# Performance work log

Hardware: AMD Instinct MI355X
Metric: run time of the kernel (lower is better)

Reference implementation:

```python
import jax, jax.numpy as jnp
import numpy as np
from jax import lax

B, T, D_IN, D_OUT = 8, 4096, 256, 256


def setup_inputs() -> dict:
    key = jax.random.key(0)
    k1, k2, k3, k4, k5 = jax.random.split(key, 5)
    bound_in = 1.0 / np.sqrt(D_IN)
    return {
        "inputs": jax.random.normal(k1, (B, T, D_IN), dtype=jnp.float32),
        "mask": jnp.zeros((B, T, 1), dtype=jnp.float32),
        "W_in": jax.random.uniform(k2, (D_OUT, D_IN), jnp.float32, -bound_in, bound_in),
        "b_in": jax.random.uniform(k3, (D_OUT,), jnp.float32, -bound_in, bound_in),
        "W_f": jax.random.uniform(k4, (D_OUT, D_IN), jnp.float32, -bound_in, bound_in),
        "b_f": jax.random.uniform(k5, (D_OUT,), jnp.float32, -bound_in, bound_in),
    }


def _forget_mult(f, x):
    # h_t = f_t * x_t + (1 - f_t) * h_{t-1}, h_{-1} = 0 (torchqrnn ForgetMult, hidden_init=None)
    fT = jnp.swapaxes(f, 0, 1)  # (T, B, D)
    xT = jnp.swapaxes(x, 0, 1)

    def step(h, fx):
        ft, xt = fx
        h = ft * xt + (1.0 - ft) * h
        return h, h

    h0 = jnp.zeros(xT.shape[1:], dtype=x.dtype)  # (B, D)
    _, hs = lax.scan(step, h0, (fT, xT))
    return jnp.swapaxes(hs, 0, 1)  # (B, T, D)


def reference(inputs, mask, W_in, b_in, W_f, b_f):
    # right_to_left = False -> no flips
    x = jnp.tanh(jnp.einsum("btd,od->bto", inputs, W_in) + b_in)
    f = jax.nn.sigmoid(jnp.einsum("btd,od->bto", inputs, W_f) + b_f + mask * 10000.0)
    return _forget_mult(f, x)
```

## Files before the change

### kernel.cpp

```cpp
#include <hip/hip_runtime.h>
#include <math.h>


typedef _Float16 f16x8 __attribute__((ext_vector_type(8)));
typedef float f32x4 __attribute__((ext_vector_type(4)));
typedef float f32x16 __attribute__((ext_vector_type(16)));

constexpr int B_ = 8, T_ = 4096, D_ = 256, K_ = 256;
constexpr int M_ = B_ * T_;
constexpr int CHUNK = 64;
constexpr int NCH = T_ / CHUNK;

struct alignas(4) XF { _Float16 x, f; };

__device__ __forceinline__ float fexp2(float a) { return __builtin_amdgcn_exp2f(a); }
__device__ __forceinline__ float frcp(float a) { return __builtin_amdgcn_rcpf(a); }
constexpr float L2E = 1.4426950408889634f;

__device__ __forceinline__ float fast_sigmoid(float z) {
  return frcp(1.f + fexp2(-z * L2E));
}
__device__ __forceinline__ float fast_tanh(float z) {
  const float t = fexp2(-2.f * L2E * fabsf(z));
  return copysignf((1.f - t) * frcp(1.f + t), z);
}

__global__ __launch_bounds__(256) void wconv(const float* __restrict__ Win,
                                             const float* __restrict__ Wf,
                                             _Float16* __restrict__ Wh2) {
  const int t = blockIdx.x * 256 + threadIdx.x;
  const int n = t & 255;
  const int kc = (t >> 8) & 3;
  const int mat = (t >> 10) & 1;
  const int kk = t >> 11;
  const float* s = (mat ? Wf : Win) + (size_t)n * K_ + kk * 32 + kc * 8;
  f32x4 a = *(const f32x4*)s;
  f32x4 b = *(const f32x4*)(s + 4);
  f16x8 o;
  o[0] = (_Float16)a[0]; o[1] = (_Float16)a[1];
  o[2] = (_Float16)a[2]; o[3] = (_Float16)a[3];
  o[4] = (_Float16)b[0]; o[5] = (_Float16)b[1];
  o[6] = (_Float16)b[2]; o[7] = (_Float16)b[3];
  *(f16x8*)(Wh2 + (size_t)t * 8) = o;
}

__global__ __launch_bounds__(256, 2) void gemm_fused(
    const float* __restrict__ A, const _Float16* __restrict__ Wh2,
    const float* __restrict__ bin, const float* __restrict__ bfv,
    const float* __restrict__ mask, XF* __restrict__ xf,
    float* __restrict__ Ap, float* __restrict__ Hp) {
  __shared__ __align__(16) char smem[65536];
  char* ldsA = smem;
  char* ldsW = smem + 32768;

  const int tid = threadIdx.x;
  const int w = tid >> 6, lane = tid & 63;
  const int mw = w >> 1, nw = w & 1;
  const int nl = lane & 31, kh = lane >> 5;
  const int ml = mw * 32 + nl;
  const int g = blockIdx.x;
  const int row0b = g * CHUNK;

  f32x16 acc[2][4];
#pragma unroll
  for (int mat = 0; mat < 2; ++mat)
#pragma unroll
    for (int nt = 0; nt < 4; ++nt) acc[mat][nt] = (f32x16)(0.f);

  {
    const int am = tid >> 2;
    const int ak4 = (tid & 3) * 8;
    const float* agp = A + (size_t)(row0b + am) * K_ + ak4 * 8;
#pragma unroll
    for (int j = 0; j < 8; ++j) {
      const int kcg = ak4 + j;
      f32x4 lo = *(const f32x4*)(agp + j * 8);
      f32x4 hi = *(const f32x4*)(agp + j * 8 + 4);
      f16x8 t;
      t[0] = (_Float16)lo[0]; t[1] = (_Float16)lo[1];
      t[2] = (_Float16)lo[2]; t[3] = (_Float16)lo[3];
      t[4] = (_Float16)hi[0]; t[5] = (_Float16)hi[1];
      t[6] = (_Float16)hi[2]; t[7] = (_Float16)hi[3];
      *(f16x8*)(ldsA + am * 512 + ((kcg ^ (am & 31)) << 4)) = t;
    }
  }

  f16x8 wreg[8];
#pragma unroll
  for (int j = 0; j < 8; ++j)
    wreg[j] = *(const f16x8*)(Wh2 + (size_t)(j * 256 + tid) * 8);

  for (int kk = 0; kk < 8; ++kk) {
#pragma unroll
    for (int j = 0; j < 8; ++j)
      *(f16x8*)(ldsW + (size_t)(j * 256 + tid) * 16) = wreg[j];
    __syncthreads();
    if (kk < 7) {
#pragma unroll
      for (int j = 0; j < 8; ++j)
        wreg[j] = *(const f16x8*)(Wh2 + (size_t)(kk + 1) * 16384 +
                                  (size_t)(j * 256 + tid) * 8);
    }
    f16x8 afr[2];
#pragma unroll
    for (int i2 = 0; i2 < 2; ++i2) {
      const int kcg = kk * 4 + i2 * 2 + kh;
      afr[i2] = *(const f16x8*)(ldsA + ml * 512 + ((kcg ^ (ml & 31)) << 4));
    }
#pragma unroll
    for (int mat = 0; mat < 2; ++mat)
#pragma unroll
      for (int nt = 0; nt < 4; ++nt) {
        const int n = nw * 128 + nt * 32 + nl;
#pragma unroll
        for (int i2 = 0; i2 < 2; ++i2) {
          const int kc = i2 * 2 + kh;
          f16x8 bfr = *(const f16x8*)(ldsW + (size_t)((mat * 4 + kc) * 256 + n) * 16);
          acc[mat][nt] = __builtin_amdgcn_mfma_f32_32x32x16_f16(
              afr[i2], bfr, acc[mat][nt], 0, 0, 0);
        }
      }
    __syncthreads();
  }

  float bx[4], bf[4];
#pragma unroll
  for (int nt = 0; nt < 4; ++nt) {
    const int col = nw * 128 + nt * 32 + nl;
    bx[nt] = bin[col];
    bf[nt] = bfv[col];
  }
  float madd[16];
  int rowl[16];
#pragma unroll
  for (int reg = 0; reg < 16; ++reg) {
    const int rl = mw * 32 + (reg & 3) + 8 * (reg >> 2) + 4 * kh;
    rowl[reg] = rl;
    madd[reg] = 10000.f * mask[row0b + rl];
  }
#pragma unroll
  for (int nt = 0; nt < 4; ++nt) {
    const int col = nw * 128 + nt * 32 + nl;
#pragma unroll
    for (int reg = 0; reg < 16; ++reg) {
      const float zx = acc[0][nt][reg] + bx[nt];
      const float zf = acc[1][nt][reg] + bf[nt] + madd[reg];
      XF v;
      v.x = (_Float16)fast_tanh(zx);
      v.f = (_Float16)fast_sigmoid(zf);
      *(XF*)(smem + ((size_t)rowl[reg] * D_ + col) * 4) = v;
      xf[((size_t)row0b + rowl[reg]) * D_ + col] = v;
    }
  }
  __syncthreads();

  const int d = tid;
  float Aa = 1.f, h = 0.f;
#pragma unroll 8
  for (int t = 0; t < CHUNK; ++t) {
    const XF v = *(const XF*)(smem + ((size_t)t * D_ + d) * 4);
    const float f = (float)v.f;
    const float a = 1.f - f;
    h = f * (float)v.x + a * h;
    Aa *= a;
  }
  Ap[(size_t)g * D_ + d] = Aa;
  Hp[(size_t)g * D_ + d] = h;
}

__global__ __launch_bounds__(256) void scan_final(const XF* __restrict__ xf,
                                                  const float* __restrict__ Ap,
                                                  const float* __restrict__ Hp,
                                                  float* __restrict__ out) {
  const int g = blockIdx.x;
  const int b = g >> 6, c = g & 63;
  const int d = threadIdx.x;
  const float* ap = Ap + ((size_t)b * NCH) * D_ + d;
  const float* hp = Hp + ((size_t)b * NCH) * D_ + d;
  float h = 0.f;
  for (int j = 0; j < c; ++j) h = hp[(size_t)j * D_] + ap[(size_t)j * D_] * h;

  const size_t base = (size_t)g * CHUNK * D_ + d;
#pragma unroll 8
  for (int t = 0; t < CHUNK; ++t) {
    const XF v = xf[base + (size_t)t * D_];
    const float f = (float)v.f;
    h = f * (float)v.x + (1.f - f) * h;
    out[base + (size_t)t * D_] = h;
  }
}

extern "C" void kernel_launch(void* const* d_in, const int* in_sizes, int n_in,
                              void* d_out, int out_size, void* d_ws, size_t ws_size,
                              hipStream_t stream) {
  const float* inputs = (const float*)d_in[0];
  const float* mask   = (const float*)d_in[1];
  const float* W_in   = (const float*)d_in[2];
  const float* b_in   = (const float*)d_in[3];
  const float* W_f    = (const float*)d_in[4];
  const float* b_f    = (const float*)d_in[5];
  float* out = (float*)d_out;
  char* ws = (char*)d_ws;

  constexpr size_t XFSZ = (size_t)M_ * D_ * sizeof(XF);
  constexpr size_t WSZ  = (size_t)2 * 256 * 256 * 2;
  constexpr size_t SUM  = (size_t)M_ / CHUNK * D_ * sizeof(float);

  XF* xf = (XF*)ws;
  _Float16* Wh2 = (_Float16*)(ws + XFSZ);
  float* Ap = (float*)(ws + XFSZ + WSZ);
  float* Hp = Ap + SUM / sizeof(float);

  wconv<<<64, 256, 0, stream>>>(W_in, W_f, Wh2);
  gemm_fused<<<512, 256, 0, stream>>>(inputs, Wh2, b_in, b_f, mask, xf, Ap, Hp);
  scan_final<<<512, 256, 0, stream>>>(xf, Ap, Hp, out);
}
```

Measured before the change: 129.9 us.

## Fuse chunk scan into GEMM kernel with cross-block flag-based carry propagation

Merges the separate scan_final kernel into the GEMM kernel. Each block publishes its chunk summary (decay product and partial state) with atomic stores and a release flag, waits on the flags of earlier chunks in the same batch, then rebuilds its carry-in and writes the output straight from LDS. This removes the fp16 x/f intermediate round trip through global memory and one kernel launch. In exchange it adds a memset, spin-waiting that relies on all 512 blocks being co-resident or scheduled in order, and serial latency along each batch's chain of chunks.

```diff
diff --git a/kernel.cpp b/kernel.cpp
--- a/kernel.cpp
+++ b/kernel.cpp
@@ -10,6 +10,7 @@
 constexpr int M_ = B_ * T_;
 constexpr int CHUNK = 64;
 constexpr int NCH = T_ / CHUNK;
+constexpr int NBLK = M_ / CHUNK;
 
 struct alignas(4) XF { _Float16 x, f; };
 
@@ -44,11 +45,11 @@
   *(f16x8*)(Wh2 + (size_t)t * 8) = o;
 }
 
-__global__ __launch_bounds__(256, 2) void gemm_fused(
+__global__ __launch_bounds__(256, 2) void gemm_scan(
     const float* __restrict__ A, const _Float16* __restrict__ Wh2,
     const float* __restrict__ bin, const float* __restrict__ bfv,
-    const float* __restrict__ mask, XF* __restrict__ xf,
-    float* __restrict__ Ap, float* __restrict__ Hp) {
+    const float* __restrict__ mask, unsigned long long* __restrict__ AH,
+    int* __restrict__ flags, float* __restrict__ out) {
   __shared__ __align__(16) char smem[65536];
   char* ldsA = smem;
   char* ldsW = smem + 32768;
@@ -149,41 +150,53 @@
       v.x = (_Float16)fast_tanh(zx);
       v.f = (_Float16)fast_sigmoid(zf);
       *(XF*)(smem + ((size_t)rowl[reg] * D_ + col) * 4) = v;
-      xf[((size_t)row0b + rowl[reg]) * D_ + col] = v;
     }
   }
   __syncthreads();
 
   const int d = tid;
-  float Aa = 1.f, h = 0.f;
+  {
+    float Aa = 1.f, h = 0.f;
+#pragma unroll 8
+    for (int t = 0; t < CHUNK; ++t) {
+      const XF v = *(const XF*)(smem + ((size_t)t * D_ + d) * 4);
+      const float f = (float)v.f;
+      const float a = 1.f - f;
+      h = f * (float)v.x + a * h;
+      Aa *= a;
+    }
+    union { float f2[2]; unsigned long long u; } pk;
+    pk.f2[0] = Aa; pk.f2[1] = h;
+    __hip_atomic_store(AH + (size_t)g * D_ + d, pk.u, __ATOMIC_RELAXED,
+                       __HIP_MEMORY_SCOPE_AGENT);
+  }
+  __syncthreads();
+  if (tid == 0)
+    __hip_atomic_store(flags + g, 1, __ATOMIC_RELEASE, __HIP_MEMORY_SCOPE_AGENT);
+
+  const int b = g >> 6, c = g & 63;
+  const int s0 = b << 6;
+  if (tid < c) {
+    while (__hip_atomic_load(flags + s0 + tid, __ATOMIC_ACQUIRE,
+                             __HIP_MEMORY_SCOPE_AGENT) == 0)
+      __builtin_amdgcn_s_sleep(8);
+  }
+  __syncthreads();
+
+  float h = 0.f;
+  for (int j = s0; j < g; ++j) {
+    unsigned long long u = __hip_atomic_load(AH + (size_t)j * D_ + d,
+                                             __ATOMIC_RELAXED,
+                                             __HIP_MEMORY_SCOPE_AGENT);
+    union { unsigned long long u; float f2[2]; } pk;
+    pk.u = u;
+    h = pk.f2[1] + pk.f2[0] * h;
+  }
+
+  const size_t base = (size_t)row0b * D_ + d;
 #pragma unroll 8
   for (int t = 0; t < CHUNK; ++t) {
     const XF v = *(const XF*)(smem + ((size_t)t * D_ + d) * 4);
-    const float f = (float)v.f;
-    const float a = 1.f - f;
-    h = f * (float)v.x + a * h;
-    Aa *= a;
-  }
-  Ap[(size_t)g * D_ + d] = Aa;
-  Hp[(size_t)g * D_ + d] = h;
-}
-
-__global__ __launch_bounds__(256) void scan_final(const XF* __restrict__ xf,
-                                                  const float* __restrict__ Ap,
-                                                  const float* __restrict__ Hp,
-                                                  float* __restrict__ out) {
-  const int g = blockIdx.x;
-  const int b = g >> 6, c = g & 63;
-  const int d = threadIdx.x;
-  const float* ap = Ap + ((size_t)b * NCH) * D_ + d;
-  const float* hp = Hp + ((size_t)b * NCH) * D_ + d;
-  float h = 0.f;
-  for (int j = 0; j < c; ++j) h = hp[(size_t)j * D_] + ap[(size_t)j * D_] * h;
-
-  const size_t base = (size_t)g * CHUNK * D_ + d;
-#pragma unroll 8
-  for (int t = 0; t < CHUNK; ++t) {
-    const XF v = xf[base + (size_t)t * D_];
     const float f = (float)v.f;
     h = f * (float)v.x + (1.f - f) * h;
     out[base + (size_t)t * D_] = h;
@@ -202,16 +215,15 @@
   float* out = (float*)d_out;
   char* ws = (char*)d_ws;
 
-  constexpr size_t XFSZ = (size_t)M_ * D_ * sizeof(XF);
-  constexpr size_t WSZ  = (size_t)2 * 256 * 256 * 2;
-  constexpr size_t SUM  = (size_t)M_ / CHUNK * D_ * sizeof(float);
-
-  XF* xf = (XF*)ws;
-  _Float16* Wh2 = (_Float16*)(ws + XFSZ);
-  float* Ap = (float*)(ws + XFSZ + WSZ);
-  float* Hp = Ap + SUM / sizeof(float);
-
+  constexpr size_t WSZ = (size_t)2 * 256 * 256 * 2;
+  constexpr size_t AHSZ = (size_t)NBLK * D_ * 8;
+
+  _Float16* Wh2 = (_Float16*)ws;
+  unsigned long long* AH = (unsigned long long*)(ws + WSZ);
+  int* flags = (int*)(ws + WSZ + AHSZ);
+
+  hipMemsetAsync(flags, 0, NBLK * sizeof(int), stream);
   wconv<<<64, 256, 0, stream>>>(W_in, W_f, Wh2);
-  gemm_fused<<<512, 256, 0, stream>>>(inputs, Wh2, b_in, b_f, mask, xf, Ap, Hp);
-  scan_final<<<512, 256, 0, stream>>>(xf, Ap, Hp, out);
-}
+  gemm_scan<<<NBLK, 256, 0, stream>>>(inputs, Wh2, b_in, b_f, mask, AH, flags,
+                                      out);
+}
```

Measured after the change: 136.9 us. +5.4%, slower.

## Shrink GEMM tile to 32 rows and read weights straight from global memory

Applied to the files above, without the earlier changes.

The fused GEMM now handles 32 rows per block instead of 64, which doubles the grid to 1024 blocks. The weight fragments are loaded straight from global memory (L2/L1) rather than staged through LDS with double-buffered registers. LDS use is halved and the occupancy hint rises to 3 blocks per CU, meant to improve latency hiding and parallelism. The trade-off is redundant weight reads per block. The final scan must also chain twice as many chunk summaries per block, since each 64-step output chunk now has two 32-row partial summaries.

```diff
diff --git a/kernel.cpp b/kernel.cpp
--- a/kernel.cpp
+++ b/kernel.cpp
@@ -8,6 +8,8 @@
 
 constexpr int B_ = 8, T_ = 4096, D_ = 256, K_ = 256;
 constexpr int M_ = B_ * T_;
+constexpr int GROWS = 32;
+constexpr int NGB = M_ / GROWS;
 constexpr int CHUNK = 64;
 constexpr int NCH = T_ / CHUNK;
 
@@ -44,36 +46,33 @@
   *(f16x8*)(Wh2 + (size_t)t * 8) = o;
 }
 
-__global__ __launch_bounds__(256, 2) void gemm_fused(
+__global__ __launch_bounds__(256, 3) void gemm32(
     const float* __restrict__ A, const _Float16* __restrict__ Wh2,
     const float* __restrict__ bin, const float* __restrict__ bfv,
     const float* __restrict__ mask, XF* __restrict__ xf,
     float* __restrict__ Ap, float* __restrict__ Hp) {
-  __shared__ __align__(16) char smem[65536];
+  __shared__ __align__(16) char smem[32768];
   char* ldsA = smem;
-  char* ldsW = smem + 32768;
 
   const int tid = threadIdx.x;
   const int w = tid >> 6, lane = tid & 63;
-  const int mw = w >> 1, nw = w & 1;
   const int nl = lane & 31, kh = lane >> 5;
-  const int ml = mw * 32 + nl;
   const int g = blockIdx.x;
-  const int row0b = g * CHUNK;
-
-  f32x16 acc[2][4];
+  const int row0 = g * GROWS;
+
+  f32x16 acc[2][2];
 #pragma unroll
   for (int mat = 0; mat < 2; ++mat)
 #pragma unroll
-    for (int nt = 0; nt < 4; ++nt) acc[mat][nt] = (f32x16)(0.f);
+    for (int nt = 0; nt < 2; ++nt) acc[mat][nt] = (f32x16)(0.f);
 
   {
-    const int am = tid >> 2;
-    const int ak4 = (tid & 3) * 8;
-    const float* agp = A + (size_t)(row0b + am) * K_ + ak4 * 8;
-#pragma unroll
-    for (int j = 0; j < 8; ++j) {
-      const int kcg = ak4 + j;
+    const int am = tid >> 3;
+    const int kb = (tid & 7) * 4;
+    const float* agp = A + (size_t)(row0 + am) * K_ + kb * 8;
+#pragma unroll
+    for (int j = 0; j < 4; ++j) {
+      const int kcg = kb + j;
       f32x4 lo = *(const f32x4*)(agp + j * 8);
       f32x4 hi = *(const f32x4*)(agp + j * 8 + 4);
       f16x8 t;
@@ -81,52 +80,40 @@
       t[2] = (_Float16)lo[2]; t[3] = (_Float16)lo[3];
       t[4] = (_Float16)hi[0]; t[5] = (_Float16)hi[1];
       t[6] = (_Float16)hi[2]; t[7] = (_Float16)hi[3];
-      *(f16x8*)(ldsA + am * 512 + ((kcg ^ (am & 31)) << 4)) = t;
+      *(f16x8*)(ldsA + am * 512 + ((kcg ^ am) << 4)) = t;
     }
   }
-
-  f16x8 wreg[8];
-#pragma unroll
-  for (int j = 0; j < 8; ++j)
-    wreg[j] = *(const f16x8*)(Wh2 + (size_t)(j * 256 + tid) * 8);
-
+  __syncthreads();
+
+#pragma unroll 2
   for (int kk = 0; kk < 8; ++kk) {
-#pragma unroll
-    for (int j = 0; j < 8; ++j)
-      *(f16x8*)(ldsW + (size_t)(j * 256 + tid) * 16) = wreg[j];
-    __syncthreads();
-    if (kk < 7) {
-#pragma unroll
-      for (int j = 0; j < 8; ++j)
-        wreg[j] = *(const f16x8*)(Wh2 + (size_t)(kk + 1) * 16384 +
-                                  (size_t)(j * 256 + tid) * 8);
-    }
     f16x8 afr[2];
 #pragma unroll
     for (int i2 = 0; i2 < 2; ++i2) {
       const int kcg = kk * 4 + i2 * 2 + kh;
-      afr[i2] = *(const f16x8*)(ldsA + ml * 512 + ((kcg ^ (ml & 31)) << 4));
+      afr[i2] = *(const f16x8*)(ldsA + nl * 512 + ((kcg ^ nl) << 4));
     }
 #pragma unroll
     for (int mat = 0; mat < 2; ++mat)
 #pragma unroll
-      for (int nt = 0; nt < 4; ++nt) {
-        const int n = nw * 128 + nt * 32 + nl;
+      for (int nt = 0; nt < 2; ++nt) {
+        const int n = w * 64 + nt * 32 + nl;
 #pragma unroll
         for (int i2 = 0; i2 < 2; ++i2) {
           const int kc = i2 * 2 + kh;
-          f16x8 bfr = *(const f16x8*)(ldsW + (size_t)((mat * 4 + kc) * 256 + n) * 16);
+          f16x8 bfr = *(const f16x8*)(Wh2 + (size_t)kk * 16384 +
+                                      (size_t)((mat * 4 + kc) * 256 + n) * 8);
           acc[mat][nt] = __builtin_amdgcn_mfma_f32_32x32x16_f16(
               afr[i2], bfr, acc[mat][nt], 0, 0, 0);
         }
       }
-    __syncthreads();
-  }
-
-  float bx[4], bf[4];
-#pragma unroll
-  for (int nt = 0; nt < 4; ++nt) {
-    const int col = nw * 128 + nt * 32 + nl;
+  }
+  __syncthreads();
+
+  float bx[2], bf[2];
+#pragma unroll
+  for (int nt = 0; nt < 2; ++nt) {
+    const int col = w * 64 + nt * 32 + nl;
     bx[nt] = bin[col];
     bf[nt] = bfv[col];
   }
@@ -134,13 +121,13 @@
   int rowl[16];
 #pragma unroll
   for (int reg = 0; reg < 16; ++reg) {
-    const int rl = mw * 32 + (reg & 3) + 8 * (reg >> 2) + 4 * kh;
+    const int rl = (reg & 3) + 8 * (reg >> 2) + 4 * kh;
     rowl[reg] = rl;
-    madd[reg] = 10000.f * mask[row0b + rl];
-  }
-#pragma unroll
-  for (int nt = 0; nt < 4; ++nt) {
-    const int col = nw * 128 + nt * 32 + nl;
+    madd[reg] = 10000.f * mask[row0 + rl];
+  }
+#pragma unroll
+  for (int nt = 0; nt < 2; ++nt) {
+    const int col = w * 64 + nt * 32 + nl;
 #pragma unroll
     for (int reg = 0; reg < 16; ++reg) {
       const float zx = acc[0][nt][reg] + bx[nt];
@@ -149,7 +136,7 @@
       v.x = (_Float16)fast_tanh(zx);
       v.f = (_Float16)fast_sigmoid(zf);
       *(XF*)(smem + ((size_t)rowl[reg] * D_ + col) * 4) = v;
-      xf[((size_t)row0b + rowl[reg]) * D_ + col] = v;
+      xf[((size_t)row0 + rowl[reg]) * D_ + col] = v;
     }
   }
   __syncthreads();
@@ -157,7 +144,7 @@
   const int d = tid;
   float Aa = 1.f, h = 0.f;
 #pragma unroll 8
-  for (int t = 0; t < CHUNK; ++t) {
+  for (int t = 0; t < GROWS; ++t) {
     const XF v = *(const XF*)(smem + ((size_t)t * D_ + d) * 4);
     const float f = (float)v.f;
     const float a = 1.f - f;
@@ -175,10 +162,12 @@
   const int g = blockIdx.x;
   const int b = g >> 6, c = g & 63;
   const int d = threadIdx.x;
-  const float* ap = Ap + ((size_t)b * NCH) * D_ + d;
-  const float* hp = Hp + ((size_t)b * NCH) * D_ + d;
+  const size_t s0 = ((size_t)b << 7) * D_ + d;
+  const int nj = 2 * c;
   float h = 0.f;
-  for (int j = 0; j < c; ++j) h = hp[(size_t)j * D_] + ap[(size_t)j * D_] * h;
+#pragma unroll 4
+  for (int j = 0; j < nj; ++j)
+    h = Hp[s0 + (size_t)j * D_] + Ap[s0 + (size_t)j * D_] * h;
 
   const size_t base = (size_t)g * CHUNK * D_ + d;
 #pragma unroll 8
@@ -204,7 +193,7 @@
 
   constexpr size_t XFSZ = (size_t)M_ * D_ * sizeof(XF);
   constexpr size_t WSZ  = (size_t)2 * 256 * 256 * 2;
-  constexpr size_t SUM  = (size_t)M_ / CHUNK * D_ * sizeof(float);
+  constexpr size_t SUM  = (size_t)NGB * D_ * sizeof(float);
 
   XF* xf = (XF*)ws;
   _Float16* Wh2 = (_Float16*)(ws + XFSZ);
@@ -212,6 +201,6 @@
   float* Hp = Ap + SUM / sizeof(float);
 
   wconv<<<64, 256, 0, stream>>>(W_in, W_f, Wh2);
-  gemm_fused<<<512, 256, 0, stream>>>(inputs, Wh2, b_in, b_f, mask, xf, Ap, Hp);
+  gemm32<<<NGB, 256, 0, stream>>>(inputs, Wh2, b_in, b_f, mask, xf, Ap, Hp);
   scan_final<<<512, 256, 0, stream>>>(xf, Ap, Hp, out);
 }
```

New measurement: 138.3 us. +6.5%, slower.

## Store per-chunk local scan and decay products, finish with affine fixup kernel

Applied to the files above, without the earlier changes.

The GEMM kernel now runs the in-chunk forget-mult scan itself. For each timestep it stores fp16 local state h and cumulative decay product P instead of raw x/f, so the final kernel only computes out = h + P*h0 with vectorized loads and no serial recurrence. A separate scan_mid kernel carries chunk boundary states per batch, replacing the O(c) prefix loop each block used to redo. LDS drops to 48KB with half-size weight slices to allow 3 blocks per CU. The cost is storing the decay product in fp16, which can underflow and lose precision over long chunks, plus an extra serial kernel launch.

```diff
diff --git a/kernel.cpp b/kernel.cpp
--- a/kernel.cpp
+++ b/kernel.cpp
@@ -5,13 +5,18 @@
 typedef _Float16 f16x8 __attribute__((ext_vector_type(8)));
 typedef float f32x4 __attribute__((ext_vector_type(4)));
 typedef float f32x16 __attribute__((ext_vector_type(16)));
+typedef unsigned int u32x4 __attribute__((ext_vector_type(4)));
 
 constexpr int B_ = 8, T_ = 4096, D_ = 256, K_ = 256;
 constexpr int M_ = B_ * T_;
 constexpr int CHUNK = 64;
 constexpr int NCH = T_ / CHUNK;
+constexpr int NBLK = M_ / CHUNK;
+constexpr int SLICE_EL = 8192;
 
 struct alignas(4) XF { _Float16 x, f; };
+struct alignas(4) HP2 { _Float16 h, p; };
+union UHP { unsigned int u; HP2 hp; XF xf; };
 
 __device__ __forceinline__ float fexp2(float a) { return __builtin_amdgcn_exp2f(a); }
 __device__ __forceinline__ float frcp(float a) { return __builtin_amdgcn_rcpf(a); }
@@ -30,10 +35,10 @@
                                              _Float16* __restrict__ Wh2) {
   const int t = blockIdx.x * 256 + threadIdx.x;
   const int n = t & 255;
-  const int kc = (t >> 8) & 3;
-  const int mat = (t >> 10) & 1;
-  const int kk = t >> 11;
-  const float* s = (mat ? Wf : Win) + (size_t)n * K_ + kk * 32 + kc * 8;
+  const int kc = (t >> 8) & 1;
+  const int mat = (t >> 9) & 1;
+  const int kk2 = t >> 10;
+  const float* s = (mat ? Wf : Win) + (size_t)n * K_ + kk2 * 16 + kc * 8;
   f32x4 a = *(const f32x4*)s;
   f32x4 b = *(const f32x4*)(s + 4);
   f16x8 o;
@@ -44,12 +49,12 @@
   *(f16x8*)(Wh2 + (size_t)t * 8) = o;
 }
 
-__global__ __launch_bounds__(256, 2) void gemm_fused(
+__global__ __launch_bounds__(256, 3) void gemm_hp(
     const float* __restrict__ A, const _Float16* __restrict__ Wh2,
     const float* __restrict__ bin, const float* __restrict__ bfv,
-    const float* __restrict__ mask, XF* __restrict__ xf,
+    const float* __restrict__ mask, unsigned int* __restrict__ HPout,
     float* __restrict__ Ap, float* __restrict__ Hp) {
-  __shared__ __align__(16) char smem[65536];
+  __shared__ __align__(16) char smem[49152];
   char* ldsA = smem;
   char* ldsW = smem + 32768;
 
@@ -59,7 +64,7 @@
   const int nl = lane & 31, kh = lane >> 5;
   const int ml = mw * 32 + nl;
   const int g = blockIdx.x;
-  const int row0b = g * CHUNK;
+  const int row0 = g * CHUNK;
 
   f32x16 acc[2][4];
 #pragma unroll
@@ -70,7 +75,7 @@
   {
     const int am = tid >> 2;
     const int ak4 = (tid & 3) * 8;
-    const float* agp = A + (size_t)(row0b + am) * K_ + ak4 * 8;
+    const float* agp = A + (size_t)(row0 + am) * K_ + ak4 * 8;
 #pragma unroll
     for (int j = 0; j < 8; ++j) {
       const int kcg = ak4 + j;
@@ -84,41 +89,37 @@
       *(f16x8*)(ldsA + am * 512 + ((kcg ^ (am & 31)) << 4)) = t;
     }
   }
-
-  f16x8 wreg[8];
-#pragma unroll
-  for (int j = 0; j < 8; ++j)
+  __syncthreads();
+
+  f16x8 wreg[4];
+#pragma unroll
+  for (int j = 0; j < 4; ++j)
     wreg[j] = *(const f16x8*)(Wh2 + (size_t)(j * 256 + tid) * 8);
 
-  for (int kk = 0; kk < 8; ++kk) {
-#pragma unroll
-    for (int j = 0; j < 8; ++j)
+  for (int kk2 = 0; kk2 < 16; ++kk2) {
+#pragma unroll
+    for (int j = 0; j < 4; ++j)
       *(f16x8*)(ldsW + (size_t)(j * 256 + tid) * 16) = wreg[j];
-    __syncthreads();
-    if (kk < 7) {
-#pragma unroll
-      for (int j = 0; j < 8; ++j)
-        wreg[j] = *(const f16x8*)(Wh2 + (size_t)(kk + 1) * 16384 +
+    if (kk2 < 15) {
+#pragma unroll
+      for (int j = 0; j < 4; ++j)
+        wreg[j] = *(const f16x8*)(Wh2 + (size_t)(kk2 + 1) * SLICE_EL +
                                   (size_t)(j * 256 + tid) * 8);
     }
-    f16x8 afr[2];
-#pragma unroll
-    for (int i2 = 0; i2 < 2; ++i2) {
-      const int kcg = kk * 4 + i2 * 2 + kh;
-      afr[i2] = *(const f16x8*)(ldsA + ml * 512 + ((kcg ^ (ml & 31)) << 4));
+    __syncthreads();
+    f16x8 afr;
+    {
+      const int kcg = kk2 * 2 + kh;
+      afr = *(const f16x8*)(ldsA + ml * 512 + ((kcg ^ (ml & 31)) << 4));
     }
 #pragma unroll
     for (int mat = 0; mat < 2; ++mat)
 #pragma unroll
       for (int nt = 0; nt < 4; ++nt) {
         const int n = nw * 128 + nt * 32 + nl;
-#pragma unroll
-        for (int i2 = 0; i2 < 2; ++i2) {
-          const int kc = i2 * 2 + kh;
-          f16x8 bfr = *(const f16x8*)(ldsW + (size_t)((mat * 4 + kc) * 256 + n) * 16);
-          acc[mat][nt] = __builtin_amdgcn_mfma_f32_32x32x16_f16(
-              afr[i2], bfr, acc[mat][nt], 0, 0, 0);
-        }
+        f16x8 bfr = *(const f16x8*)(ldsW + (size_t)((mat * 2 + kh) * 256 + n) * 16);
+        acc[mat][nt] = __builtin_amdgcn_mfma_f32_32x32x16_f16(
+            afr, bfr, acc[mat][nt], 0, 0, 0);
       }
     __syncthreads();
   }
@@ -131,62 +132,92 @@
     bf[nt] = bfv[col];
   }
   float madd[16];
-  int rowl[16];
 #pragma unroll
   for (int reg = 0; reg < 16; ++reg) {
     const int rl = mw * 32 + (reg & 3) + 8 * (reg >> 2) + 4 * kh;
-    rowl[reg] = rl;
-    madd[reg] = 10000.f * mask[row0b + rl];
-  }
-#pragma unroll
-  for (int nt = 0; nt < 4; ++nt) {
-    const int col = nw * 128 + nt * 32 + nl;
-#pragma unroll
-    for (int reg = 0; reg < 16; ++reg) {
-      const float zx = acc[0][nt][reg] + bx[nt];
-      const float zf = acc[1][nt][reg] + bf[nt] + madd[reg];
-      XF v;
-      v.x = (_Float16)fast_tanh(zx);
-      v.f = (_Float16)fast_sigmoid(zf);
-      *(XF*)(smem + ((size_t)rowl[reg] * D_ + col) * 4) = v;
-      xf[((size_t)row0b + rowl[reg]) * D_ + col] = v;
-    }
-  }
-  __syncthreads();
+    madd[reg] = 10000.f * mask[row0 + rl];
+  }
 
   const int d = tid;
-  float Aa = 1.f, h = 0.f;
+  float hrun = 0.f, Prun = 1.f;
+#pragma unroll
+  for (int p = 0; p < 2; ++p) {
+    if (mw == p) {
+#pragma unroll
+      for (int nt = 0; nt < 4; ++nt) {
+        const int col = nw * 128 + nt * 32 + nl;
+#pragma unroll
+        for (int reg = 0; reg < 16; ++reg) {
+          const int rloc = (reg & 3) + 8 * (reg >> 2) + 4 * kh;
+          const float zx = acc[0][nt][reg] + bx[nt];
+          const float zf = acc[1][nt][reg] + bf[nt] + madd[reg];
+          XF v;
+          v.x = (_Float16)fast_tanh(zx);
+          v.f = (_Float16)fast_sigmoid(zf);
+          *(XF*)(smem + ((size_t)rloc * D_ + col) * 4) = v;
+        }
+      }
+    }
+    __syncthreads();
 #pragma unroll 8
-  for (int t = 0; t < CHUNK; ++t) {
-    const XF v = *(const XF*)(smem + ((size_t)t * D_ + d) * 4);
-    const float f = (float)v.f;
-    const float a = 1.f - f;
-    h = f * (float)v.x + a * h;
-    Aa *= a;
-  }
-  Ap[(size_t)g * D_ + d] = Aa;
-  Hp[(size_t)g * D_ + d] = h;
-}
-
-__global__ __launch_bounds__(256) void scan_final(const XF* __restrict__ xf,
-                                                  const float* __restrict__ Ap,
-                                                  const float* __restrict__ Hp,
-                                                  float* __restrict__ out) {
+    for (int t = 0; t < 32; ++t) {
+      char* slot = smem + ((size_t)t * D_ + d) * 4;
+      const XF v = *(const XF*)slot;
+      const float f = (float)v.f;
+      const float a = 1.f - f;
+      hrun = f * (float)v.x + a * hrun;
+      Prun *= a;
+      HP2 o;
+      o.h = (_Float16)hrun;
+      o.p = (_Float16)Prun;
+      *(HP2*)slot = o;
+    }
+    __syncthreads();
+#pragma unroll
+    for (int j = 0; j < 8; ++j) {
+      const int c = j * 256 + tid;
+      u32x4 vv = *(const u32x4*)(smem + (size_t)c * 16);
+      *(u32x4*)(HPout + (size_t)g * 16384 + (size_t)p * 8192 + (size_t)c * 4) = vv;
+    }
+    __syncthreads();
+  }
+
+  Ap[(size_t)g * D_ + d] = Prun;
+  Hp[(size_t)g * D_ + d] = hrun;
+}
+
+__global__ __launch_bounds__(256) void scan_mid(const float* __restrict__ Ap,
+                                                const float* __restrict__ Hp,
+                                                float* __restrict__ hs) {
+  const int b = blockIdx.x, d = threadIdx.x;
+  float h = 0.f;
+#pragma unroll 8
+  for (int c = 0; c < NCH; ++c) {
+    const size_t i = ((size_t)(b * NCH + c)) * D_ + d;
+    hs[i] = h;
+    h = Hp[i] + Ap[i] * h;
+  }
+}
+
+__global__ __launch_bounds__(256) void final_k(const unsigned int* __restrict__ HP,
+                                               const float* __restrict__ hs,
+                                               float* __restrict__ out) {
   const int g = blockIdx.x;
-  const int b = g >> 6, c = g & 63;
-  const int d = threadIdx.x;
-  const float* ap = Ap + ((size_t)b * NCH) * D_ + d;
-  const float* hp = Hp + ((size_t)b * NCH) * D_ + d;
-  float h = 0.f;
-  for (int j = 0; j < c; ++j) h = hp[(size_t)j * D_] + ap[(size_t)j * D_] * h;
-
-  const size_t base = (size_t)g * CHUNK * D_ + d;
-#pragma unroll 8
-  for (int t = 0; t < CHUNK; ++t) {
-    const XF v = xf[base + (size_t)t * D_];
-    const float f = (float)v.f;
-    h = f * (float)v.x + (1.f - f) * h;
-    out[base + (size_t)t * D_] = h;
+  const int lane = threadIdx.x & 63, wv = threadIdx.x >> 6;
+  const int d0 = lane * 4;
+  const f32x4 h0 = *(const f32x4*)(hs + (size_t)g * D_ + d0);
+#pragma unroll 4
+  for (int tt = 0; tt < 16; ++tt) {
+    const int t = wv * 16 + tt;
+    const size_t idx = ((size_t)g * CHUNK + t) * D_ + d0;
+    u32x4 u = *(const u32x4*)(HP + idx);
+    f32x4 o;
+#pragma unroll
+    for (int i = 0; i < 4; ++i) {
+      UHP q; q.u = u[i];
+      o[i] = (float)q.hp.h + (float)q.hp.p * h0[i];
+    }
+    *(f32x4*)(out + idx) = o;
   }
 }
 
@@ -202,16 +233,18 @@
   float* out = (float*)d_out;
   char* ws = (char*)d_ws;
 
-  constexpr size_t XFSZ = (size_t)M_ * D_ * sizeof(XF);
+  constexpr size_t HPSZ = (size_t)M_ * D_ * 4;
   constexpr size_t WSZ  = (size_t)2 * 256 * 256 * 2;
-  constexpr size_t SUM  = (size_t)M_ / CHUNK * D_ * sizeof(float);
-
-  XF* xf = (XF*)ws;
-  _Float16* Wh2 = (_Float16*)(ws + XFSZ);
-  float* Ap = (float*)(ws + XFSZ + WSZ);
-  float* Hp = Ap + SUM / sizeof(float);
+  constexpr size_t SUM  = (size_t)NBLK * D_ * sizeof(float);
+
+  unsigned int* HPb = (unsigned int*)ws;
+  _Float16* Wh2 = (_Float16*)(ws + HPSZ);
+  float* Ap = (float*)(ws + HPSZ + WSZ);
+  float* Hp = (float*)(ws + HPSZ + WSZ + SUM);
+  float* hs = (float*)(ws + HPSZ + WSZ + 2 * SUM);
 
   wconv<<<64, 256, 0, stream>>>(W_in, W_f, Wh2);
-  gemm_fused<<<512, 256, 0, stream>>>(inputs, Wh2, b_in, b_f, mask, xf, Ap, Hp);
-  scan_final<<<512, 256, 0, stream>>>(xf, Ap, Hp, out);
-}
+  gemm_hp<<<NBLK, 256, 0, stream>>>(inputs, Wh2, b_in, b_f, mask, HPb, Ap, Hp);
+  scan_mid<<<B_, 256, 0, stream>>>(Ap, Hp, hs);
+  final_k<<<NBLK, 256, 0, stream>>>(HPb, hs, out);
+}
```

Result: no change. 128.0 us (-1.4%).
